# Performance work log

Hardware: AMD Instinct MI355X
Metric: run time of the kernel (lower is better)

The kernel has to match this reference:

```python
import jax, jax.numpy as jnp
import numpy as np

B, Q, K, D, H = 4, 2048, 2048, 512, 8
DH = D // H
MASK_VAL = -1e6


def setup_inputs() -> dict:
    key = jax.random.key(0)
    ks = jax.random.split(key, 8)
    queries = jax.random.normal(ks[0], (B, Q, D), dtype=jnp.float32)
    keys = jax.random.normal(ks[1], (B, K, D), dtype=jnp.float32)
    values = jax.random.normal(ks[2], (B, K, D), dtype=jnp.float32)
    valid_lens = jax.random.randint(ks[3], (B,), 1, K + 1, dtype=jnp.int32)
    # torch nn.Linear weights: shape [out_features, in_features], y = x @ W.T
    s = 1.0 / np.sqrt(D)
    W_q = jax.random.uniform(ks[4], (D, D), jnp.float32, -s, s)
    W_k = jax.random.uniform(ks[5], (D, D), jnp.float32, -s, s)
    W_v = jax.random.uniform(ks[6], (D, D), jnp.float32, -s, s)
    W_o = jax.random.uniform(ks[7], (D, D), jnp.float32, -s, s)
    return {"queries": queries, "keys": keys, "values": values,
            "valid_lens": valid_lens, "W_q": W_q, "W_k": W_k,
            "W_v": W_v, "W_o": W_o}


def _split_heads(x):
    # [B, S, D] -> [B, H, S, DH]
    b, s, _ = x.shape
    return x.reshape(b, s, H, DH).transpose(0, 2, 1, 3)


def reference(queries, keys, values, valid_lens, W_q, W_k, W_v, W_o):
    q = _split_heads(queries @ W_q.T)   # [B,H,Q,DH]
    k = _split_heads(keys @ W_k.T)      # [B,H,K,DH]
    v = _split_heads(values @ W_v.T)    # [B,H,K,DH]
    scores = jnp.einsum("bhqd,bhkd->bhqk", q, k) / jnp.sqrt(jnp.float32(DH))
    # padding mask: key position < valid_len[b], broadcast over heads & queries
    mask = jnp.arange(K)[None, None, None, :] < valid_lens[:, None, None, None]
    scores = jnp.where(mask, scores, MASK_VAL)
    attn = jax.nn.softmax(scores, axis=-1)  # dropout=eval/no-op
    out = jnp.einsum("bhqk,bhkd->bhqd", attn, v)
    out = out.transpose(0, 2, 1, 3).reshape(queries.shape[0], q.shape[2], D)
    return out @ W_o.T
```

## Files before the change

### kernel.cpp

```cpp
#include <hip/hip_runtime.h>
#include <cstdint>
#include <cstddef>

#define BB  4
#define QQ  2048
#define SK  2048
#define DD  512
#define HH  8
#define DHH 64

typedef __bf16 bf16;
typedef bf16  bf16x8 __attribute__((ext_vector_type(8)));
typedef bf16  bf16x4 __attribute__((ext_vector_type(4)));
typedef float f32x4  __attribute__((ext_vector_type(4)));
typedef uint32_t u32x4 __attribute__((ext_vector_type(4)));

__device__ __forceinline__ void async16(void* lds, const void* g) {
  __builtin_amdgcn_global_load_lds(
      (const __attribute__((address_space(1))) unsigned int*)g,
      (__attribute__((address_space(3))) unsigned int*)lds, 16, 0, 0);
}

__device__ __forceinline__ uint32_t pk2(float lo, float hi) {
  return __builtin_amdgcn_perm(__builtin_bit_cast(uint32_t, hi),
                               __builtin_bit_cast(uint32_t, lo), 0x07060302u);
}

__global__ __launch_bounds__(256) void cvt_w(
    const float* __restrict__ w0, const float* __restrict__ w1,
    const float* __restrict__ w2, const float* __restrict__ w3,
    bf16* __restrict__ d0, bf16* __restrict__ d1, bf16* __restrict__ d2,
    bf16* __restrict__ d3, int nw4) {
  int i = blockIdx.x * 256 + threadIdx.x;
  const float* s;
  bf16* d;
  if (i < nw4)             { s = w0; d = d0; }
  else if (i < 2 * nw4)    { s = w1; d = d1; i -= nw4; }
  else if (i < 3 * nw4)    { s = w2; d = d2; i -= 2 * nw4; }
  else if (i < 4 * nw4)    { s = w3; d = d3; i -= 3 * nw4; }
  else return;
  float4 vv = ((const float4*)s)[i];
  bf16x4 o;
  o[0] = (bf16)vv.x; o[1] = (bf16)vv.y; o[2] = (bf16)vv.z; o[3] = (bf16)vv.w;
  ((bf16x4*)d)[i] = o;
}

template <int XSIDE, bool XF32, typename XT, typename EpiF>
__device__ __forceinline__ void gemm64(
    bf16* __restrict__ lW, bf16* __restrict__ lX,
    const bf16* __restrict__ W, const XT* __restrict__ X,
    int tW, int tX, EpiF epi_fn) {
  const int tid  = threadIdx.x;
  const int l    = tid & 63;
  const int w    = tid >> 6;
  const int lrow = l & 15, lq = l >> 4, rx = lrow & 7;
  const int wm = (w >> 1) * 32, wn = (w & 1) * 32;

  float4 rg[4];
  auto loadXraw = [&](int it) {
    if constexpr (XF32) {
      const int kt = it * 64;
#pragma unroll
      for (int j = 0; j < 2; ++j) {
        int c = j * 256 + tid, row = c >> 3, gcc = (c & 7) ^ (row & 7);
        const float* s = &X[(size_t)(tX + row) * DD + kt + gcc * 8];
        rg[2 * j]     = *(const float4*)s;
        rg[2 * j + 1] = *(const float4*)(s + 4);
      }
    }
  };

  f32x4 acc[2][2] = {};
  if constexpr (XF32) loadXraw(0);
  for (int it = 0; it < 8; ++it) {
    const int kt = it * 64;
    if (it) __syncthreads();
#pragma unroll
    for (int j = 0; j < 2; ++j) {
      int c = j * 256 + tid, row = c >> 3, gcc = (c & 7) ^ (row & 7);
      async16(&lW[c * 8], &W[(size_t)(tW + row) * DD + kt + gcc * 8]);
    }
    if constexpr (XF32) {
#pragma unroll
      for (int j = 0; j < 2; ++j) {
        int c = j * 256 + tid;
        float4 a = rg[2 * j], b = rg[2 * j + 1];
        bf16x8 o;
        o[0] = (bf16)a.x; o[1] = (bf16)a.y; o[2] = (bf16)a.z; o[3] = (bf16)a.w;
        o[4] = (bf16)b.x; o[5] = (bf16)b.y; o[6] = (bf16)b.z; o[7] = (bf16)b.w;
        *(bf16x8*)&lX[c * 8] = o;
      }
    } else {
#pragma unroll
      for (int j = 0; j < 2; ++j) {
        int c = j * 256 + tid, row = c >> 3, gcc = (c & 7) ^ (row & 7);
        async16(&lX[c * 8], &X[(size_t)(tX + row) * DD + kt + gcc * 8]);
      }
    }
    __syncthreads();
    if constexpr (XF32) {
      if (it + 1 < 8) loadXraw(it + 1);
    }
    const bf16* bufA = XSIDE ? lW : lX;
    const bf16* bufB = XSIDE ? lX : lW;
#pragma unroll
    for (int ks = 0; ks < 2; ++ks) {
      bf16x8 afr[2], bfr[2];
#pragma unroll
      for (int t = 0; t < 2; ++t) {
        int ra = wm + t * 16 + lrow, rb = wn + t * 16 + lrow;
        afr[t] = *(const bf16x8*)&bufA[(ra * 8 + ((ks * 4 + lq) ^ rx)) * 8];
        bfr[t] = *(const bf16x8*)&bufB[(rb * 8 + ((ks * 4 + lq) ^ rx)) * 8];
      }
#pragma unroll
      for (int mt = 0; mt < 2; ++mt)
#pragma unroll
        for (int nt = 0; nt < 2; ++nt)
          acc[mt][nt] = __builtin_amdgcn_mfma_f32_16x16x32_bf16(
              afr[mt], bfr[nt], acc[mt][nt], 0, 0, 0);
    }
  }

  const int tM = XSIDE ? tW : tX, tN = XSIDE ? tX : tW;
#pragma unroll
  for (int mt = 0; mt < 2; ++mt)
#pragma unroll
    for (int nt = 0; nt < 2; ++nt)
      epi_fn(acc[mt][nt], tM + wm + mt * 16 + lq * 4, tN + wn + nt * 16 + lrow);
}

__global__ __launch_bounds__(256, 5) void proj3(
    const float* __restrict__ xq, const bf16* __restrict__ wq, bf16* __restrict__ qh,
    const float* __restrict__ xk, const bf16* __restrict__ wk, bf16* __restrict__ kh,
    const float* __restrict__ xv, const bf16* __restrict__ wv, bf16* __restrict__ vt,
    float qscale) {
  __shared__ __align__(16) bf16 lW[64 * 64];
  __shared__ __align__(16) bf16 lX[64 * 64];
  const int z = blockIdx.y, x = blockIdx.x;
  const int tW = (x >> 7) * 64, tX = (x & 127) * 64;
  if (z < 2) {
    const bf16*  W = z == 0 ? wq : wk;
    const float* Xf = z == 0 ? xq : xk;
    bf16* Cout     = z == 0 ? qh : kh;
    const float scale = z == 0 ? qscale : 1.0f;
    gemm64<1, true>(lW, lX, W, Xf, tW, tX,
                    [&](const f32x4& a, int row0, int col) {
      int b2 = col >> 11, s = col & 2047;
      int h2 = row0 >> 6, dh0 = row0 & 63;
      bf16x4 o;
#pragma unroll
      for (int r = 0; r < 4; ++r) o[r] = (bf16)(a[r] * scale);
      *(bf16x4*)&Cout[((size_t)(b2 * HH + h2) * QQ + s) * DHH + dh0] = o;
    });
  } else {
    gemm64<0, true>(lW, lX, wv, xv, tW, tX,
                    [&](const f32x4& a, int row0, int col) {
      int b2 = row0 >> 11, s0 = row0 & 2047;
      int h2 = col >> 6,  dh = col & 63;
      int tile = s0 >> 6, kk = s0 & 63;
      int g = kk >> 4, a2 = (kk >> 2) & 3;
      int idx0 = ((g >> 1) * 4 + a2) * 8 + (g & 1) * 4;
      bf16x4 o;
#pragma unroll
      for (int r = 0; r < 4; ++r) o[r] = (bf16)a[r];
      *(bf16x4*)&vt[((size_t)(b2 * HH + h2) * DHH + dh) * SK + tile * 64 + idx0] = o;
    });
  }
}

__global__ __launch_bounds__(256, 4) void proj_o(
    const bf16* __restrict__ wo, const bf16* __restrict__ ao,
    float* __restrict__ Cout) {
  __shared__ __align__(16) bf16 lW[64 * 64];
  __shared__ __align__(16) bf16 lX[64 * 64];
  const int x = blockIdx.x;
  const int tW = (x >> 7) * 64, tX = (x & 127) * 64;
  gemm64<1, false>(lW, lX, wo, ao, tW, tX,
                   [&](const f32x4& a, int row0, int col) {
    *(float4*)&Cout[(size_t)col * DD + row0] = *(const float4*)&a;
  });
}

__global__ __launch_bounds__(256, 3) void attn_fused(
    const bf16* __restrict__ qh, const bf16* __restrict__ kh,
    const bf16* __restrict__ vt, const int* __restrict__ valid_lens,
    bf16* __restrict__ ao) {
  __shared__ __align__(16) bf16 lK[3][64 * 64];
  __shared__ __align__(16) bf16 lV[3][64 * 64];
  const int tid  = threadIdx.x;
  const int l    = tid & 63;
  const int w    = tid >> 6;
  const int lrow = l & 15, lq = l >> 4;
  const int rx   = lrow & 7;
  const int bh = blockIdx.x;
  const int b = bh >> 3, h = bh & 7;
  const int qt = blockIdx.y;
  const int vl  = valid_lens[b];
  const int nkt = (vl + 63) >> 6;

  const int q0 = qt * 128 + w * 32;
  const bf16* qbase = qh + (size_t)bh * QQ * DHH;
  const bf16* kbase = kh + (size_t)bh * SK * DHH;
  const bf16* vbase = vt + (size_t)bh * DHH * SK;

  auto stageKV = [&](int k0, int buf) {
#pragma unroll
    for (int j = 0; j < 2; ++j) {
      int c = j * 256 + tid, row = c >> 3, gcc = (c & 7) ^ (row & 7);
      async16(&lK[buf][c * 8], &kbase[(size_t)(k0 + row) * DHH + gcc * 8]);
    }
#pragma unroll
    for (int j = 0; j < 2; ++j) {
      int c = j * 256 + tid, row = c >> 3, gcc = (c & 7) ^ (row & 7);
      async16(&lV[buf][c * 8], &vbase[(size_t)row * SK + k0 + gcc * 8]);
    }
  };

  bf16x8 qf[2][2];
#pragma unroll
  for (int g = 0; g < 2; ++g)
#pragma unroll
    for (int ks = 0; ks < 2; ++ks)
      qf[g][ks] = *(const bf16x8*)
          &qbase[(size_t)(q0 + g * 16 + lrow) * DHH + ks * 32 + lq * 8];

  f32x4 acc[2][4] = {};
  float rs[2] = {0.f, 0.f};

  stageKV(0, 0);
  asm volatile("s_waitcnt vmcnt(0)" ::: "memory");

  for (int kt = 0; kt < nkt; ++kt) {
    const int bi = kt % 3;
    if (kt + 1 < nkt) {
      stageKV((kt + 1) * 64, (kt + 1) % 3);
      asm volatile("s_waitcnt vmcnt(4)" ::: "memory");
    } else {
      asm volatile("s_waitcnt vmcnt(0)" ::: "memory");
    }
    __builtin_amdgcn_s_barrier();
    asm volatile("" ::: "memory");
    const bf16* bufK = lK[bi];
    const bf16* bufV = lV[bi];
    const int k0 = kt * 64;

    f32x4 s[2][4] = {};
    __builtin_amdgcn_s_setprio(1);
#pragma unroll
    for (int ks = 0; ks < 2; ++ks) {
#pragma unroll
      for (int t = 0; t < 4; ++t) {
        int row = t * 16 + lrow;
        int chunkc = row * 8 + ((ks * 4 + lq) ^ rx);
        bf16x8 kf = *(const bf16x8*)&bufK[chunkc * 8];
#pragma unroll
        for (int g = 0; g < 2; ++g)
          s[g][t] = __builtin_amdgcn_mfma_f32_16x16x32_bf16(
              kf, qf[g][ks], s[g][t], 0, 0, 0);
      }
    }
    __builtin_amdgcn_s_setprio(0);

    if (vl < k0 + 64) {
#pragma unroll
      for (int t = 0; t < 4; ++t) {
        int kb = k0 + t * 16 + lq * 4;
#pragma unroll
        for (int r = 0; r < 4; ++r)
          if (kb + r >= vl) { s[0][t][r] = -1e30f; s[1][t][r] = -1e30f; }
      }
    }

#pragma unroll
    for (int g = 0; g < 2; ++g)
#pragma unroll
      for (int t = 0; t < 4; ++t)
#pragma unroll
        for (int r = 0; r < 4; ++r) {
          float p = __builtin_amdgcn_exp2f(s[g][t][r]);
          rs[g] += p;
          s[g][t][r] = p;
        }

#pragma unroll
    for (int p2 = 0; p2 < 2; ++p2) {
      u32x4 pu[2];
#pragma unroll
      for (int g = 0; g < 2; ++g) {
        pu[g][0] = pk2(s[g][2 * p2][0], s[g][2 * p2][1]);
        pu[g][1] = pk2(s[g][2 * p2][2], s[g][2 * p2][3]);
        pu[g][2] = pk2(s[g][2 * p2 + 1][0], s[g][2 * p2 + 1][1]);
        pu[g][3] = pk2(s[g][2 * p2 + 1][2], s[g][2 * p2 + 1][3]);
      }
      bf16x8 pb0 = __builtin_bit_cast(bf16x8, pu[0]);
      bf16x8 pb1 = __builtin_bit_cast(bf16x8, pu[1]);
      int cc = (p2 * 4 + lq) ^ rx;
      __builtin_amdgcn_s_setprio(1);
#pragma unroll
      for (int mt = 0; mt < 4; ++mt) {
        int row = mt * 16 + lrow;
        bf16x8 vf = *(const bf16x8*)&bufV[(row * 8 + cc) * 8];
        acc[0][mt] = __builtin_amdgcn_mfma_f32_16x16x32_bf16(
            vf, pb0, acc[0][mt], 0, 0, 0);
        acc[1][mt] = __builtin_amdgcn_mfma_f32_16x16x32_bf16(
            vf, pb1, acc[1][mt], 0, 0, 0);
      }
      __builtin_amdgcn_s_setprio(0);
    }
  }

#pragma unroll
  for (int g = 0; g < 2; ++g) {
    rs[g] += __shfl_xor(rs[g], 16);
    rs[g] += __shfl_xor(rs[g], 32);
  }

#pragma unroll
  for (int g = 0; g < 2; ++g) {
    float inv = 1.0f / rs[g];
    int q = q0 + g * 16 + lrow;
#pragma unroll
    for (int mt = 0; mt < 4; ++mt) {
      bf16x4 o;
#pragma unroll
      for (int r = 0; r < 4; ++r) o[r] = (bf16)(acc[g][mt][r] * inv);
      *(bf16x4*)&ao[((size_t)(b * QQ + q)) * DD + h * DHH + mt * 16 + lq * 4] = o;
    }
  }
}

extern "C" void kernel_launch(void* const* d_in, const int* in_sizes, int n_in,
                              void* d_out, int out_size, void* d_ws, size_t ws_size,
                              hipStream_t stream) {
  const float* queries    = (const float*)d_in[0];
  const float* keys       = (const float*)d_in[1];
  const float* values     = (const float*)d_in[2];
  const int*   valid_lens = (const int*)d_in[3];
  const float* W_q = (const float*)d_in[4];
  const float* W_k = (const float*)d_in[5];
  const float* W_v = (const float*)d_in[6];
  const float* W_o = (const float*)d_in[7];

  const size_t NX = (size_t)BB * QQ * DD;
  const size_t NW = (size_t)DD * DD;

  bf16* wq = (bf16*)d_ws;
  bf16* wk = wq + NW;
  bf16* wv = wk + NW;
  bf16* wo = wv + NW;
  bf16* qh = wo + NW;
  bf16* kh = qh + NX;
  bf16* vt = kh + NX;
  bf16* ao = vt + NX;

  dim3 blk(256);
  const int nw4 = (int)(NW / 4);
  cvt_w<<<dim3((4 * nw4 + 255) / 256), blk, 0, stream>>>(
      W_q, W_k, W_v, W_o, wq, wk, wv, wo, nw4);

  const float qscale = 0.125f * 1.44269504088896340736f;
  proj3<<<dim3(1024, 3), blk, 0, stream>>>(queries, wq, qh, keys, wk, kh,
                                           values, wv, vt, qscale);

  attn_fused<<<dim3(BB * HH, QQ / 128), blk, 0, stream>>>(
      qh, kh, vt, valid_lens, ao);

  proj_o<<<dim3(1024), blk, 0, stream>>>(wo, ao, (float*)d_out);
}
```

Measured before the change: 174.8 us.

## Pipeline projection GEMMs with triple-buffered W in LDS and register-resident X

Rewrites the shared projection GEMM helper. Weight tiles now go through a three-slot LDS ring filled with async loads, with a single barrier per k-step gated on vmcnt. Activation fragments are loaded straight from global memory into double-buffered registers in MFMA layout, so X no longer passes through LDS. The aim is to overlap global loads with MFMA work and to remove one of the two barriers and the X round trip through LDS. In exchange it uses more registers, which is reflected in proj3's launch bounds dropping from 5 to 4 blocks. The X global loads are also less coalesced, and each wave reloads X rows that other waves share.

```diff
diff --git a/kernel.cpp b/kernel.cpp
--- a/kernel.cpp
+++ b/kernel.cpp
@@ -46,96 +46,112 @@
 }
 
 template <int XSIDE, bool XF32, typename XT, typename EpiF>
-__device__ __forceinline__ void gemm64(
-    bf16* __restrict__ lW, bf16* __restrict__ lX,
-    const bf16* __restrict__ W, const XT* __restrict__ X,
-    int tW, int tX, EpiF epi_fn) {
+__device__ __forceinline__ void gemm64p(
+    bf16* __restrict__ lW3, const bf16* __restrict__ W,
+    const XT* __restrict__ X, int tW, int tX, EpiF epi_fn) {
   const int tid  = threadIdx.x;
   const int l    = tid & 63;
   const int w    = tid >> 6;
   const int lrow = l & 15, lq = l >> 4, rx = lrow & 7;
   const int wm = (w >> 1) * 32, wn = (w & 1) * 32;
-
-  float4 rg[4];
-  auto loadXraw = [&](int it) {
-    if constexpr (XF32) {
-      const int kt = it * 64;
-#pragma unroll
-      for (int j = 0; j < 2; ++j) {
-        int c = j * 256 + tid, row = c >> 3, gcc = (c & 7) ^ (row & 7);
-        const float* s = &X[(size_t)(tX + row) * DD + kt + gcc * 8];
-        rg[2 * j]     = *(const float4*)s;
-        rg[2 * j + 1] = *(const float4*)(s + 4);
-      }
-    }
-  };
-
-  f32x4 acc[2][2] = {};
-  if constexpr (XF32) loadXraw(0);
-  for (int it = 0; it < 8; ++it) {
+  const int wW = XSIDE ? wm : wn;
+  const int wX = XSIDE ? wn : wm;
+  constexpr int BS = XF32 ? 10 : 6;
+
+  float4 rg[2][8];
+  bf16x8 xbr[2][4];
+
+  auto stageW = [&](int it) {
+    bf16* dst = lW3 + (it % 3) * 4096;
     const int kt = it * 64;
-    if (it) __syncthreads();
 #pragma unroll
     for (int j = 0; j < 2; ++j) {
       int c = j * 256 + tid, row = c >> 3, gcc = (c & 7) ^ (row & 7);
-      async16(&lW[c * 8], &W[(size_t)(tW + row) * DD + kt + gcc * 8]);
-    }
-    if constexpr (XF32) {
-#pragma unroll
-      for (int j = 0; j < 2; ++j) {
-        int c = j * 256 + tid;
-        float4 a = rg[2 * j], b = rg[2 * j + 1];
-        bf16x8 o;
-        o[0] = (bf16)a.x; o[1] = (bf16)a.y; o[2] = (bf16)a.z; o[3] = (bf16)a.w;
-        o[4] = (bf16)b.x; o[5] = (bf16)b.y; o[6] = (bf16)b.z; o[7] = (bf16)b.w;
-        *(bf16x8*)&lX[c * 8] = o;
-      }
+      async16(&dst[c * 8], &W[(size_t)(tW + row) * DD + kt + gcc * 8]);
+    }
+  };
+  auto loadX = [&](int it) {
+    const int kt = it * 64, pp = it & 1;
+#pragma unroll
+    for (int ks = 0; ks < 2; ++ks)
+#pragma unroll
+      for (int t = 0; t < 2; ++t) {
+        const XT* p = &X[(size_t)(tX + wX + t * 16 + lrow) * DD
+                         + kt + ks * 32 + lq * 8];
+        if constexpr (XF32) {
+          rg[pp][(ks * 2 + t) * 2]     = *(const float4*)p;
+          rg[pp][(ks * 2 + t) * 2 + 1] = *(const float4*)(p + 4);
+        } else {
+          xbr[pp][ks * 2 + t] = *(const bf16x8*)p;
+        }
+      }
+  };
+
+  f32x4 acc[2][2] = {};
+  stageW(0);
+  loadX(0);
+#pragma unroll
+  for (int it = 0; it < 8; ++it) {
+    if (it + 1 < 8) {
+      stageW(it + 1);
+      loadX(it + 1);
+      asm volatile("s_waitcnt vmcnt(%0)" :: "i"(BS) : "memory");
     } else {
-#pragma unroll
-      for (int j = 0; j < 2; ++j) {
-        int c = j * 256 + tid, row = c >> 3, gcc = (c & 7) ^ (row & 7);
-        async16(&lX[c * 8], &X[(size_t)(tX + row) * DD + kt + gcc * 8]);
-      }
-    }
-    __syncthreads();
-    if constexpr (XF32) {
-      if (it + 1 < 8) loadXraw(it + 1);
-    }
-    const bf16* bufA = XSIDE ? lW : lX;
-    const bf16* bufB = XSIDE ? lX : lW;
+      asm volatile("s_waitcnt vmcnt(0)" ::: "memory");
+    }
+    __builtin_amdgcn_s_barrier();
+    asm volatile("" ::: "memory");
+
+    const bf16* buf = lW3 + (it % 3) * 4096;
+    const int pp = it & 1;
+    bf16x8 xf[2][2];
+#pragma unroll
+    for (int ks = 0; ks < 2; ++ks)
+#pragma unroll
+      for (int t = 0; t < 2; ++t) {
+        if constexpr (XF32) {
+          float4 a = rg[pp][(ks * 2 + t) * 2];
+          float4 b = rg[pp][(ks * 2 + t) * 2 + 1];
+          bf16x8 o;
+          o[0] = (bf16)a.x; o[1] = (bf16)a.y; o[2] = (bf16)a.z; o[3] = (bf16)a.w;
+          o[4] = (bf16)b.x; o[5] = (bf16)b.y; o[6] = (bf16)b.z; o[7] = (bf16)b.w;
+          xf[ks][t] = o;
+        } else {
+          xf[ks][t] = xbr[pp][ks * 2 + t];
+        }
+      }
 #pragma unroll
     for (int ks = 0; ks < 2; ++ks) {
-      bf16x8 afr[2], bfr[2];
+      bf16x8 wf[2];
 #pragma unroll
       for (int t = 0; t < 2; ++t) {
-        int ra = wm + t * 16 + lrow, rb = wn + t * 16 + lrow;
-        afr[t] = *(const bf16x8*)&bufA[(ra * 8 + ((ks * 4 + lq) ^ rx)) * 8];
-        bfr[t] = *(const bf16x8*)&bufB[(rb * 8 + ((ks * 4 + lq) ^ rx)) * 8];
+        int row = wW + t * 16 + lrow;
+        wf[t] = *(const bf16x8*)&buf[(row * 8 + ((ks * 4 + lq) ^ rx)) * 8];
       }
 #pragma unroll
       for (int mt = 0; mt < 2; ++mt)
 #pragma unroll
         for (int nt = 0; nt < 2; ++nt)
           acc[mt][nt] = __builtin_amdgcn_mfma_f32_16x16x32_bf16(
-              afr[mt], bfr[nt], acc[mt][nt], 0, 0, 0);
-    }
-  }
-
-  const int tM = XSIDE ? tW : tX, tN = XSIDE ? tX : tW;
+              XSIDE ? wf[mt] : xf[ks][mt], XSIDE ? xf[ks][nt] : wf[nt],
+              acc[mt][nt], 0, 0, 0);
+    }
+  }
+
+  const int tA = XSIDE ? tW : tX, tB = XSIDE ? tX : tW;
 #pragma unroll
   for (int mt = 0; mt < 2; ++mt)
 #pragma unroll
     for (int nt = 0; nt < 2; ++nt)
-      epi_fn(acc[mt][nt], tM + wm + mt * 16 + lq * 4, tN + wn + nt * 16 + lrow);
-}
-
-__global__ __launch_bounds__(256, 5) void proj3(
+      epi_fn(acc[mt][nt], tA + wm + mt * 16 + lq * 4, tB + wn + nt * 16 + lrow);
+}
+
+__global__ __launch_bounds__(256, 4) void proj3(
     const float* __restrict__ xq, const bf16* __restrict__ wq, bf16* __restrict__ qh,
     const float* __restrict__ xk, const bf16* __restrict__ wk, bf16* __restrict__ kh,
     const float* __restrict__ xv, const bf16* __restrict__ wv, bf16* __restrict__ vt,
     float qscale) {
-  __shared__ __align__(16) bf16 lW[64 * 64];
-  __shared__ __align__(16) bf16 lX[64 * 64];
+  __shared__ __align__(16) bf16 lW3[3 * 64 * 64];
   const int z = blockIdx.y, x = blockIdx.x;
   const int tW = (x >> 7) * 64, tX = (x & 127) * 64;
   if (z < 2) {
@@ -143,8 +159,8 @@
     const float* Xf = z == 0 ? xq : xk;
     bf16* Cout     = z == 0 ? qh : kh;
     const float scale = z == 0 ? qscale : 1.0f;
-    gemm64<1, true>(lW, lX, W, Xf, tW, tX,
-                    [&](const f32x4& a, int row0, int col) {
+    gemm64p<1, true>(lW3, W, Xf, tW, tX,
+                     [&](const f32x4& a, int row0, int col) {
       int b2 = col >> 11, s = col & 2047;
       int h2 = row0 >> 6, dh0 = row0 & 63;
       bf16x4 o;
@@ -153,8 +169,8 @@
       *(bf16x4*)&Cout[((size_t)(b2 * HH + h2) * QQ + s) * DHH + dh0] = o;
     });
   } else {
-    gemm64<0, true>(lW, lX, wv, xv, tW, tX,
-                    [&](const f32x4& a, int row0, int col) {
+    gemm64p<0, true>(lW3, wv, xv, tW, tX,
+                     [&](const f32x4& a, int row0, int col) {
       int b2 = row0 >> 11, s0 = row0 & 2047;
       int h2 = col >> 6,  dh = col & 63;
       int tile = s0 >> 6, kk = s0 & 63;
@@ -171,12 +187,11 @@
 __global__ __launch_bounds__(256, 4) void proj_o(
     const bf16* __restrict__ wo, const bf16* __restrict__ ao,
     float* __restrict__ Cout) {
-  __shared__ __align__(16) bf16 lW[64 * 64];
-  __shared__ __align__(16) bf16 lX[64 * 64];
+  __shared__ __align__(16) bf16 lW3[3 * 64 * 64];
   const int x = blockIdx.x;
   const int tW = (x >> 7) * 64, tX = (x & 127) * 64;
-  gemm64<1, false>(lW, lX, wo, ao, tW, tX,
-                   [&](const f32x4& a, int row0, int col) {
+  gemm64p<1, false, bf16>(lW3, wo, ao, tW, tX,
+                          [&](const f32x4& a, int row0, int col) {
     *(float4*)&Cout[(size_t)col * DD + row0] = *(const float4*)&a;
   });
 }
```

Result: slower. 238.2 us (+36.3%).

## Stage full weight slab in LDS once and stream activations from global

Applied to the files above, without the earlier changes.

Replaces the double-buffered 64x64 K-tiled projection GEMM with a version that loads a full 64x512 bf16 weight slab into LDS once per block. Activation fragments are then read directly from global memory into registers, converted to bf16 if needed, and fed to MFMA. Each block now computes two 64-row output tiles, so the grids for proj3 and proj_o are halved. This removes the per-K-step barriers and the LDS staging of activations, but it uses 64KB of LDS per block, lowers the occupancy bound, and makes activation loads uncoalesced and unhidden, with each wave reading rows at a stride.

```diff
diff --git a/kernel.cpp b/kernel.cpp
--- a/kernel.cpp
+++ b/kernel.cpp
@@ -45,106 +45,90 @@
   ((bf16x4*)d)[i] = o;
 }
 
-template <int XSIDE, bool XF32, typename XT, typename EpiF>
-__device__ __forceinline__ void gemm64(
-    bf16* __restrict__ lW, bf16* __restrict__ lX,
-    const bf16* __restrict__ W, const XT* __restrict__ X,
-    int tW, int tX, EpiF epi_fn) {
+template <int XSIDE, bool XF32, int G, typename XT, typename EpiF>
+__device__ __forceinline__ void gemm_wonce(
+    bf16* __restrict__ lW, const bf16* __restrict__ W,
+    const XT* __restrict__ X, int tW, int tX0, EpiF epi_fn) {
   const int tid  = threadIdx.x;
   const int l    = tid & 63;
   const int w    = tid >> 6;
   const int lrow = l & 15, lq = l >> 4, rx = lrow & 7;
   const int wm = (w >> 1) * 32, wn = (w & 1) * 32;
-
-  float4 rg[4];
-  auto loadXraw = [&](int it) {
-    if constexpr (XF32) {
-      const int kt = it * 64;
-#pragma unroll
-      for (int j = 0; j < 2; ++j) {
-        int c = j * 256 + tid, row = c >> 3, gcc = (c & 7) ^ (row & 7);
-        const float* s = &X[(size_t)(tX + row) * DD + kt + gcc * 8];
-        rg[2 * j]     = *(const float4*)s;
-        rg[2 * j + 1] = *(const float4*)(s + 4);
-      }
-    }
-  };
-
-  f32x4 acc[2][2] = {};
-  if constexpr (XF32) loadXraw(0);
-  for (int it = 0; it < 8; ++it) {
-    const int kt = it * 64;
-    if (it) __syncthreads();
-#pragma unroll
-    for (int j = 0; j < 2; ++j) {
-      int c = j * 256 + tid, row = c >> 3, gcc = (c & 7) ^ (row & 7);
-      async16(&lW[c * 8], &W[(size_t)(tW + row) * DD + kt + gcc * 8]);
-    }
-    if constexpr (XF32) {
-#pragma unroll
-      for (int j = 0; j < 2; ++j) {
-        int c = j * 256 + tid;
-        float4 a = rg[2 * j], b = rg[2 * j + 1];
-        bf16x8 o;
-        o[0] = (bf16)a.x; o[1] = (bf16)a.y; o[2] = (bf16)a.z; o[3] = (bf16)a.w;
-        o[4] = (bf16)b.x; o[5] = (bf16)b.y; o[6] = (bf16)b.z; o[7] = (bf16)b.w;
-        *(bf16x8*)&lX[c * 8] = o;
-      }
-    } else {
-#pragma unroll
-      for (int j = 0; j < 2; ++j) {
-        int c = j * 256 + tid, row = c >> 3, gcc = (c & 7) ^ (row & 7);
-        async16(&lX[c * 8], &X[(size_t)(tX + row) * DD + kt + gcc * 8]);
-      }
-    }
-    __syncthreads();
-    if constexpr (XF32) {
-      if (it + 1 < 8) loadXraw(it + 1);
-    }
-    const bf16* bufA = XSIDE ? lW : lX;
-    const bf16* bufB = XSIDE ? lX : lW;
-#pragma unroll
-    for (int ks = 0; ks < 2; ++ks) {
-      bf16x8 afr[2], bfr[2];
-#pragma unroll
-      for (int t = 0; t < 2; ++t) {
-        int ra = wm + t * 16 + lrow, rb = wn + t * 16 + lrow;
-        afr[t] = *(const bf16x8*)&bufA[(ra * 8 + ((ks * 4 + lq) ^ rx)) * 8];
-        bfr[t] = *(const bf16x8*)&bufB[(rb * 8 + ((ks * 4 + lq) ^ rx)) * 8];
-      }
-#pragma unroll
-      for (int mt = 0; mt < 2; ++mt)
-#pragma unroll
-        for (int nt = 0; nt < 2; ++nt)
-          acc[mt][nt] = __builtin_amdgcn_mfma_f32_16x16x32_bf16(
-              afr[mt], bfr[nt], acc[mt][nt], 0, 0, 0);
-    }
-  }
-
-  const int tM = XSIDE ? tW : tX, tN = XSIDE ? tX : tW;
-#pragma unroll
-  for (int mt = 0; mt < 2; ++mt)
-#pragma unroll
-    for (int nt = 0; nt < 2; ++nt)
-      epi_fn(acc[mt][nt], tM + wm + mt * 16 + lq * 4, tN + wn + nt * 16 + lrow);
-}
-
-__global__ __launch_bounds__(256, 5) void proj3(
+  const int wW = XSIDE ? wm : wn;
+  const int wX = XSIDE ? wn : wm;
+
+#pragma unroll
+  for (int j = 0; j < 16; ++j) {
+    int c = j * 256 + tid, s = c >> 9, cc = c & 511;
+    int row = cc >> 3, gcc = (cc & 7) ^ (row & 7);
+    async16(&lW[c * 8], &W[(size_t)(tW + row) * DD + s * 64 + gcc * 8]);
+  }
+  __syncthreads();
+
+#pragma unroll
+  for (int pg = 0; pg < G; ++pg) {
+    const int tX = tX0 + pg * 64;
+    f32x4 acc[2][2] = {};
+#pragma unroll
+    for (int kt = 0; kt < 4; ++kt) {
+#pragma unroll
+      for (int ks = 0; ks < 4; ++ks) {
+        const int kk = kt * 16 + ks * 4 + lq;
+        const int sb = (kk >> 3) * 512;
+        const int sl = (kk & 7) ^ rx;
+        bf16x8 wf[2], xf[2];
+#pragma unroll
+        for (int t = 0; t < 2; ++t) {
+          int rW = wW + t * 16 + lrow;
+          wf[t] = *(const bf16x8*)&lW[(sb + rW * 8 + sl) * 8];
+          const XT* p = &X[(size_t)(tX + wX + t * 16 + lrow) * DD
+                           + kt * 128 + ks * 32 + lq * 8];
+          if constexpr (XF32) {
+            float4 a = *(const float4*)p, b = *(const float4*)(p + 4);
+            bf16x8 o;
+            o[0] = (bf16)a.x; o[1] = (bf16)a.y;
+            o[2] = (bf16)a.z; o[3] = (bf16)a.w;
+            o[4] = (bf16)b.x; o[5] = (bf16)b.y;
+            o[6] = (bf16)b.z; o[7] = (bf16)b.w;
+            xf[t] = o;
+          } else {
+            xf[t] = *(const bf16x8*)p;
+          }
+        }
+#pragma unroll
+        for (int mt = 0; mt < 2; ++mt)
+#pragma unroll
+          for (int nt = 0; nt < 2; ++nt)
+            acc[mt][nt] = __builtin_amdgcn_mfma_f32_16x16x32_bf16(
+                XSIDE ? wf[mt] : xf[mt], XSIDE ? xf[nt] : wf[nt],
+                acc[mt][nt], 0, 0, 0);
+      }
+    }
+    const int tA = XSIDE ? tW : tX, tB = XSIDE ? tX : tW;
+#pragma unroll
+    for (int mt = 0; mt < 2; ++mt)
+#pragma unroll
+      for (int nt = 0; nt < 2; ++nt)
+        epi_fn(acc[mt][nt], tA + wm + mt * 16 + lq * 4,
+               tB + wn + nt * 16 + lrow);
+  }
+}
+
+__global__ __launch_bounds__(256, 2) void proj3(
     const float* __restrict__ xq, const bf16* __restrict__ wq, bf16* __restrict__ qh,
     const float* __restrict__ xk, const bf16* __restrict__ wk, bf16* __restrict__ kh,
     const float* __restrict__ xv, const bf16* __restrict__ wv, bf16* __restrict__ vt,
     float qscale) {
-  __shared__ __align__(16) bf16 lW[64 * 64];
-  __shared__ __align__(16) bf16 lX[64 * 64];
+  __shared__ __align__(16) bf16 lW[64 * 512];
   const int z = blockIdx.y, x = blockIdx.x;
-  const int tW = (x >> 7) * 64, tX = (x & 127) * 64;
+  const int tW = (x >> 6) * 64, tX0 = (x & 63) * 128;
   if (z < 2) {
     const bf16*  W = z == 0 ? wq : wk;
     const float* Xf = z == 0 ? xq : xk;
     bf16* Cout     = z == 0 ? qh : kh;
     const float scale = z == 0 ? qscale : 1.0f;
-    gemm64<1, true>(lW, lX, W, Xf, tW, tX,
-                    [&](const f32x4& a, int row0, int col) {
+    gemm_wonce<1, true, 2>(lW, W, Xf, tW, tX0,
+                           [&](const f32x4& a, int row0, int col) {
       int b2 = col >> 11, s = col & 2047;
       int h2 = row0 >> 6, dh0 = row0 & 63;
       bf16x4 o;
@@ -153,8 +137,8 @@
       *(bf16x4*)&Cout[((size_t)(b2 * HH + h2) * QQ + s) * DHH + dh0] = o;
     });
   } else {
-    gemm64<0, true>(lW, lX, wv, xv, tW, tX,
-                    [&](const f32x4& a, int row0, int col) {
+    gemm_wonce<0, true, 2>(lW, wv, xv, tW, tX0,
+                           [&](const f32x4& a, int row0, int col) {
       int b2 = row0 >> 11, s0 = row0 & 2047;
       int h2 = col >> 6,  dh = col & 63;
       int tile = s0 >> 6, kk = s0 & 63;
@@ -168,15 +152,14 @@
   }
 }
 
-__global__ __launch_bounds__(256, 4) void proj_o(
+__global__ __launch_bounds__(256, 2) void proj_o(
     const bf16* __restrict__ wo, const bf16* __restrict__ ao,
     float* __restrict__ Cout) {
-  __shared__ __align__(16) bf16 lW[64 * 64];
-  __shared__ __align__(16) bf16 lX[64 * 64];
+  __shared__ __align__(16) bf16 lW[64 * 512];
   const int x = blockIdx.x;
-  const int tW = (x >> 7) * 64, tX = (x & 127) * 64;
-  gemm64<1, false>(lW, lX, wo, ao, tW, tX,
-                   [&](const f32x4& a, int row0, int col) {
+  const int tW = (x >> 6) * 64, tX0 = (x & 63) * 128;
+  gemm_wonce<1, false, 2, bf16>(lW, wo, ao, tW, tX0,
+                                [&](const f32x4& a, int row0, int col) {
     *(float4*)&Cout[(size_t)col * DD + row0] = *(const float4*)&a;
   });
 }
@@ -359,11 +342,11 @@
       W_q, W_k, W_v, W_o, wq, wk, wv, wo, nw4);
 
   const float qscale = 0.125f * 1.44269504088896340736f;
-  proj3<<<dim3(1024, 3), blk, 0, stream>>>(queries, wq, qh, keys, wk, kh,
-                                           values, wv, vt, qscale);
+  proj3<<<dim3(512, 3), blk, 0, stream>>>(queries, wq, qh, keys, wk, kh,
+                                          values, wv, vt, qscale);
 
   attn_fused<<<dim3(BB * HH, QQ / 128), blk, 0, stream>>>(
       qh, kh, vt, valid_lens, ao);
 
-  proj_o<<<dim3(1024), blk, 0, stream>>>(wo, ao, (float*)d_out);
-}
+  proj_o<<<dim3(512), blk, 0, stream>>>(wo, ao, (float*)d_out);
+}
```

After: 236.4 us. 35.2% more time.
